# Kernel tuning notes

Measured on AMD Instinct MI355X. Metric: run time of the kernel, lower is better.

Reference implementation:

```python
import jax, jax.numpy as jnp
import numpy as np

T, B, L, I, H = 1024, 1024, 10, 10, 10


def setup_inputs() -> dict:
    key = jax.random.key(0)
    ks = jax.random.split(key, 7)
    scale = 1.0 / np.sqrt(H)
    x = jax.random.normal(ks[0], (T, B, I), dtype=jnp.float32)
    hp = jax.random.normal(ks[1], (L, B, H), dtype=jnp.float32)
    cp = jax.random.normal(ks[2], (L, B, H), dtype=jnp.float32)
    # torch nn.LSTM params, uniform(-1/sqrt(H), 1/sqrt(H)); layer 0 input = I == H so all layers stack
    W_ih = jax.random.uniform(ks[3], (L, 4 * H, I), minval=-scale, maxval=scale, dtype=jnp.float32)
    W_hh = jax.random.uniform(ks[4], (L, 4 * H, H), minval=-scale, maxval=scale, dtype=jnp.float32)
    b_ih = jax.random.uniform(ks[5], (L, 4 * H), minval=-scale, maxval=scale, dtype=jnp.float32)
    b_hh = jax.random.uniform(ks[6], (L, 4 * H), minval=-scale, maxval=scale, dtype=jnp.float32)
    return {"x": x, "hp": hp, "cp": cp, "W_ih": W_ih, "W_hh": W_hh, "b_ih": b_ih, "b_hh": b_hh}


def _run_layer(inp, h0, c0, Wi, Wh, bi, bh):
    # precompute input projections for all timesteps: [T, B, 4H]
    xg = jnp.einsum('tbi,gi->tbg', inp, Wi) + bi + bh

    def step(carry, xg_t):
        h, c = carry
        g = xg_t + h @ Wh.T  # [B, 4H]; torch gate order: i, f, g, o
        i_g, f_g, g_g, o_g = jnp.split(g, 4, axis=-1)
        i_g = jax.nn.sigmoid(i_g)
        f_g = jax.nn.sigmoid(f_g)
        g_g = jnp.tanh(g_g)
        o_g = jax.nn.sigmoid(o_g)
        c = f_g * c + i_g * g_g
        h = o_g * jnp.tanh(c)
        return (h, c), h

    (hT, cT), ys = jax.lax.scan(step, (h0, c0), xg)
    return ys, hT, cT


def reference(x, hp, cp, W_ih, W_hh, b_ih, b_hh):
    out = x
    hns, cns = [], []
    for l in range(hp.shape[0]):  # fixed small layer stack
        out, hn, cn = _run_layer(out, hp[l], cp[l], W_ih[l], W_hh[l], b_ih[l], b_hh[l])
        hns.append(hn)
        cns.append(cn)
    return out, jnp.stack(hns), jnp.stack(cns)
```

## Files before the change

### kernel.cpp

```cpp
#include <hip/hip_runtime.h>

namespace {

constexpr int T = 1024;
constexpr int B = 1024;
constexpr int L = 10;
constexpr int H = 10;
constexpr int NTHREADS = 128;
constexpr int U = 4;
constexpr int NWIN = T / U;
constexpr int NINT = NWIN + L - 1;
constexpr int BH = B * H;
constexpr int ROWF = 20;

using v2f = __attribute__((ext_vector_type(2))) float;
using v4f = __attribute__((ext_vector_type(4))) float;

__device__ __forceinline__ v2f v2fma(v2f a, v2f b, v2f c) {
    return __builtin_elementwise_fma(a, b, c);
}
__device__ __forceinline__ void pin2(v2f& v) { asm volatile("" : "+v"(v)); }
__device__ __forceinline__ float rcp_f(float x) { return __builtin_amdgcn_rcpf(x); }
__device__ __forceinline__ float exp2_f(float x) {
    float r; asm("v_exp_f32 %0, %1" : "=v"(r) : "v"(x)); return r;
}
__device__ __forceinline__ v2f lo2(v4f q) { return __builtin_shufflevector(q, q, 0, 1); }
__device__ __forceinline__ v2f hi2(v4f q) { return __builtin_shufflevector(q, q, 2, 3); }
#define LDS_FENCE asm volatile("" ::: "memory")

__global__
__attribute__((amdgpu_flat_work_group_size(NTHREADS, NTHREADS)))
__attribute__((amdgpu_waves_per_eu(2)))
void lstm_pipeline(const float* __restrict__ x,
                   const float* __restrict__ hp,
                   const float* __restrict__ cp,
                   const float* __restrict__ Wih,
                   const float* __restrict__ Whh,
                   const float* __restrict__ bih,
                   const float* __restrict__ bhh,
                   float* __restrict__ out,
                   float* __restrict__ hn,
                   float* __restrict__ cn)
{
    __shared__ __align__(16) float buf[2][U][L + 1][ROWF];

    const int tid = threadIdx.x;
    const int wv = tid >> 6;
    const int ln = tid & 63;
    int lidx;
    if (wv == 0) lidx = (ln < 60) ? ln : (ln - 10);
    else         lidx = (ln < 40) ? (60 + ln) : (90 + (ln - 40) % 10);
    const int l = lidx / 10;
    const int j = lidx % 10;
    const int b = blockIdx.x;
    const int boff = b * H + j;

    const float NL2E = -1.44269504088896340736f;
    v2f sA; sA[0] = NL2E;        sA[1] = NL2E;
    v2f sB; sB[0] = 2.0f * NL2E; sB[1] = NL2E;
    v2f wiA[10], wiB[10], whA[10], whB[10], bA, bB;
    {
        const float* WiL = Wih + (size_t)l * 4 * H * H;
        const float* WhL = Whh + (size_t)l * 4 * H * H;
        #pragma unroll
        for (int k = 0; k < 10; ++k) {
            v2f t;
            t[0] = WiL[(0 * H + j) * H + k]; t[1] = WiL[(1 * H + j) * H + k];
            wiA[k] = t * sA;
            t[0] = WiL[(2 * H + j) * H + k]; t[1] = WiL[(3 * H + j) * H + k];
            wiB[k] = t * sB;
            t[0] = WhL[(0 * H + j) * H + k]; t[1] = WhL[(1 * H + j) * H + k];
            whA[k] = t * sA;
            t[0] = WhL[(2 * H + j) * H + k]; t[1] = WhL[(3 * H + j) * H + k];
            whB[k] = t * sB;
        }
        const int bo = l * 4 * H;
        bA[0] = bih[bo + j] + bhh[bo + j];
        bA[1] = bih[bo + H + j] + bhh[bo + H + j];
        bB[0] = bih[bo + 2 * H + j] + bhh[bo + 2 * H + j];
        bB[1] = bih[bo + 3 * H + j] + bhh[bo + 3 * H + j];
        bA = bA * sA;
        bB = bB * sB;
    }
    #pragma unroll
    for (int k = 0; k < 10; ++k) { pin2(wiA[k]); pin2(wiB[k]); pin2(whA[k]); pin2(whB[k]); }
    pin2(bA); pin2(bB);

    float h = hp[(l * B + b) * H + j];
    float c = cp[(l * B + b) * H + j];
    {
        v2f hh; hh[0] = h; hh[1] = h;
        *(v2f*)&buf[(l + 1) & 1][U - 1][l + 1][2 * j] = hh;
    }

    const bool is_st = (lidx < 10);
    float xcur[U], xnext[U];
    if (is_st) {
        #pragma unroll
        for (int u = 0; u < U; ++u) {
            float xv = x[(size_t)u * BH + boff];
            v2f xx; xx[0] = xv; xx[1] = xv;
            *(v2f*)&buf[1][u][0][2 * j] = xx;
        }
        #pragma unroll
        for (int u = 0; u < U; ++u) xcur[u] = x[(size_t)(U + u) * BH + boff];
    }
    __syncthreads();

    v2f aA[U], aB[U];

    auto prefetchx = [&](int k) {
        if (is_st && (k + 2) < NWIN) {
            #pragma unroll
            for (int u = 0; u < U; ++u)
                xnext[u] = x[(size_t)((k + 2) * U + u) * BH + boff];
        }
    };

    auto phase1 = [&](int k, int rp) {
        const unsigned w = (unsigned)(k - l);
        if (w < (unsigned)NWIN) {
            #pragma unroll
            for (int u = 0; u < U; ++u) {
                const float* xr = &buf[rp][u][l][0];
                v4f q0 = *(const v4f*)(xr + 0);
                v4f q1 = *(const v4f*)(xr + 4);
                v4f q2 = *(const v4f*)(xr + 8);
                v4f q3 = *(const v4f*)(xr + 12);
                v4f q4 = *(const v4f*)(xr + 16);
                v2f a  = v2fma(wiA[0], lo2(q0), bA);
                v2f bv = v2fma(wiB[0], lo2(q0), bB);
                a = v2fma(wiA[1], hi2(q0), a);  bv = v2fma(wiB[1], hi2(q0), bv);
                a = v2fma(wiA[2], lo2(q1), a);  bv = v2fma(wiB[2], lo2(q1), bv);
                a = v2fma(wiA[3], hi2(q1), a);  bv = v2fma(wiB[3], hi2(q1), bv);
                a = v2fma(wiA[4], lo2(q2), a);  bv = v2fma(wiB[4], lo2(q2), bv);
                a = v2fma(wiA[5], hi2(q2), a);  bv = v2fma(wiB[5], hi2(q2), bv);
                a = v2fma(wiA[6], lo2(q3), a);  bv = v2fma(wiB[6], lo2(q3), bv);
                a = v2fma(wiA[7], hi2(q3), a);  bv = v2fma(wiB[7], hi2(q3), bv);
                a = v2fma(wiA[8], lo2(q4), a);  bv = v2fma(wiB[8], lo2(q4), bv);
                a = v2fma(wiA[9], hi2(q4), a);  bv = v2fma(wiB[9], hi2(q4), bv);
                aA[u] = a;
                aB[u] = bv;
            }
        }
    };

    auto phase2 = [&](int k, int wp, int rp) {
        const unsigned w = (unsigned)(k - l);
        if (w < (unsigned)NWIN) {
            v4f hq0 = *(const v4f*)&buf[rp][U - 1][l + 1][0];
            v4f hq1 = *(const v4f*)&buf[rp][U - 1][l + 1][4];
            v4f hq2 = *(const v4f*)&buf[rp][U - 1][l + 1][8];
            v4f hq3 = *(const v4f*)&buf[rp][U - 1][l + 1][12];
            v4f hq4 = *(const v4f*)&buf[rp][U - 1][l + 1][16];
            float hv[U];
            #pragma unroll
            for (int u = 0; u < U; ++u) {
                v4f q0, q1, q2, q3, q4;
                if (u == 0) { q0 = hq0; q1 = hq1; q2 = hq2; q3 = hq3; q4 = hq4; }
                else {
                    const float* hr = &buf[wp][u - 1][l + 1][0];
                    q0 = *(const v4f*)(hr + 0);
                    q1 = *(const v4f*)(hr + 4);
                    q2 = *(const v4f*)(hr + 8);
                    q3 = *(const v4f*)(hr + 12);
                    q4 = *(const v4f*)(hr + 16);
                }
                v2f a1 = v2fma(whA[0], lo2(q0), aA[u]);
                v2f a2 = whA[1] * hi2(q0);
                v2f b1 = v2fma(whB[0], lo2(q0), aB[u]);
                v2f b2 = whB[1] * hi2(q0);
                a1 = v2fma(whA[2], lo2(q1), a1);  a2 = v2fma(whA[3], hi2(q1), a2);
                b1 = v2fma(whB[2], lo2(q1), b1);  b2 = v2fma(whB[3], hi2(q1), b2);
                a1 = v2fma(whA[4], lo2(q2), a1);  a2 = v2fma(whA[5], hi2(q2), a2);
                b1 = v2fma(whB[4], lo2(q2), b1);  b2 = v2fma(whB[5], hi2(q2), b2);
                a1 = v2fma(whA[6], lo2(q3), a1);  a2 = v2fma(whA[7], hi2(q3), a2);
                b1 = v2fma(whB[6], lo2(q3), b1);  b2 = v2fma(whB[7], hi2(q3), b2);
                a1 = v2fma(whA[8], lo2(q4), a1);  a2 = v2fma(whA[9], hi2(q4), a2);
                b1 = v2fma(whB[8], lo2(q4), b1);  b2 = v2fma(whB[9], hi2(q4), b2);
                const v2f pA = a1 + a2;
                const v2f pB = b1 + b2;
                const float Ei = exp2_f(pA[0]);
                const float Ef = exp2_f(pA[1]);
                const float Eg = exp2_f(pB[0]);
                const float Eo = exp2_f(pB[1]);
                const float d1 = 1.0f + Ef;
                const float e1 = 1.0f + Ei;
                const float e2 = 1.0f + Eg;
                const float d2 = e1 * e2;
                const float num = fmaf(c, d2, (1.0f - Eg) * d1);
                c = num * rcp_f(d1 * d2);
                const float Ec = exp2_f((2.0f * NL2E) * c);
                const float o1 = 1.0f + Eo;
                const float o2 = 1.0f + Ec;
                h = (1.0f - Ec) * rcp_f(o1 * o2);
                v2f hh; hh[0] = h; hh[1] = h;
                *(v2f*)&buf[wp][u][l + 1][2 * j] = hh;
                hv[u] = h;
            }
            if (l == L - 1) {
                const int t0 = (int)w * U;
                #pragma unroll
                for (int u = 0; u < U; ++u)
                    out[(size_t)(t0 + u) * BH + boff] = hv[u];
            }
        }
    };

    auto stagex = [&](int k, int wp) {
        if (is_st && (k + 1) < NWIN) {
            #pragma unroll
            for (int u = 0; u < U; ++u) {
                v2f xx; xx[0] = xcur[u]; xx[1] = xcur[u];
                *(v2f*)&buf[wp][u][0][2 * j] = xx;
            }
            #pragma unroll
            for (int u = 0; u < U; ++u) xcur[u] = xnext[u];
        }
    };

    if (wv == 0) {
        for (int kk = 0; kk < NINT + 1; kk += 2) {
            prefetchx(kk);
            phase1(kk, 1);        LDS_FENCE;
            phase2(kk, 0, 1);     LDS_FENCE;
            stagex(kk, 0);
            __syncthreads();
            prefetchx(kk + 1);
            phase1(kk + 1, 0);    LDS_FENCE;
            phase2(kk + 1, 1, 0); LDS_FENCE;
            stagex(kk + 1, 1);
            __syncthreads();
        }
    } else {
        for (int kk = 0; kk < NINT + 1; kk += 2) {
            phase2(kk - 1, 1, 0); LDS_FENCE;
            phase1(kk, 1);
            __syncthreads();
            phase2(kk, 0, 1);     LDS_FENCE;
            phase1(kk + 1, 0);
            __syncthreads();
        }
    }

    hn[(l * B + b) * H + j] = h;
    cn[(l * B + b) * H + j] = c;
}

}

extern "C" void kernel_launch(void* const* d_in, const int* in_sizes, int n_in,
                              void* d_out, int out_size, void* d_ws, size_t ws_size,
                              hipStream_t stream) {
    (void)in_sizes; (void)n_in; (void)d_ws; (void)ws_size; (void)out_size;
    const float* x   = (const float*)d_in[0];
    const float* hp  = (const float*)d_in[1];
    const float* cp  = (const float*)d_in[2];
    const float* Wih = (const float*)d_in[3];
    const float* Whh = (const float*)d_in[4];
    const float* bih = (const float*)d_in[5];
    const float* bhh = (const float*)d_in[6];

    float* out = (float*)d_out;
    float* hn  = out + (size_t)T * B * H;
    float* cn  = hn + (size_t)L * B * H;

    lstm_pipeline<<<dim3(B), dim3(NTHREADS), 0, stream>>>(
        x, hp, cp, Wih, Whh, bih, bhh, out, hn, cn);
}
```

Before: 484.5 us.

## Store hidden/input rows unduplicated and split dot products along the reduction axis

```diff
diff --git a/kernel.cpp b/kernel.cpp
--- a/kernel.cpp
+++ b/kernel.cpp
@@ -11,7 +11,7 @@
 constexpr int NWIN = T / U;
 constexpr int NINT = NWIN + L - 1;
 constexpr int BH = B * H;
-constexpr int ROWF = 20;
+constexpr int ROWP = 12;
 
 using v2f = __attribute__((ext_vector_type(2))) float;
 using v4f = __attribute__((ext_vector_type(4))) float;
@@ -42,7 +42,7 @@
                    float* __restrict__ hn,
                    float* __restrict__ cn)
 {
-    __shared__ __align__(16) float buf[2][U][L + 1][ROWF];
+    __shared__ __align__(16) float buf[2][U][L + 1][ROWP];
 
     const int tid = threadIdx.x;
     const int wv = tid >> 6;
@@ -56,58 +56,48 @@
     const int boff = b * H + j;
 
     const float NL2E = -1.44269504088896340736f;
-    v2f sA; sA[0] = NL2E;        sA[1] = NL2E;
-    v2f sB; sB[0] = 2.0f * NL2E; sB[1] = NL2E;
-    v2f wiA[10], wiB[10], whA[10], whB[10], bA, bB;
+    v2f wi[4][5], wh[4][5], bias[4];
     {
         const float* WiL = Wih + (size_t)l * 4 * H * H;
         const float* WhL = Whh + (size_t)l * 4 * H * H;
-        #pragma unroll
-        for (int k = 0; k < 10; ++k) {
-            v2f t;
-            t[0] = WiL[(0 * H + j) * H + k]; t[1] = WiL[(1 * H + j) * H + k];
-            wiA[k] = t * sA;
-            t[0] = WiL[(2 * H + j) * H + k]; t[1] = WiL[(3 * H + j) * H + k];
-            wiB[k] = t * sB;
-            t[0] = WhL[(0 * H + j) * H + k]; t[1] = WhL[(1 * H + j) * H + k];
-            whA[k] = t * sA;
-            t[0] = WhL[(2 * H + j) * H + k]; t[1] = WhL[(3 * H + j) * H + k];
-            whB[k] = t * sB;
-        }
         const int bo = l * 4 * H;
-        bA[0] = bih[bo + j] + bhh[bo + j];
-        bA[1] = bih[bo + H + j] + bhh[bo + H + j];
-        bB[0] = bih[bo + 2 * H + j] + bhh[bo + 2 * H + j];
-        bB[1] = bih[bo + 3 * H + j] + bhh[bo + 3 * H + j];
-        bA = bA * sA;
-        bB = bB * sB;
+        #pragma unroll
+        for (int g = 0; g < 4; ++g) {
+            const float s = (g == 2) ? 2.0f * NL2E : NL2E;
+            const float* wr = WiL + (size_t)(g * H + j) * H;
+            const float* hr = WhL + (size_t)(g * H + j) * H;
+            #pragma unroll
+            for (int p = 0; p < 5; ++p) {
+                wi[g][p][0] = wr[2 * p] * s; wi[g][p][1] = wr[2 * p + 1] * s;
+                wh[g][p][0] = hr[2 * p] * s; wh[g][p][1] = hr[2 * p + 1] * s;
+            }
+            bias[g][0] = (bih[bo + g * H + j] + bhh[bo + g * H + j]) * s;
+            bias[g][1] = 0.0f;
+        }
     }
     #pragma unroll
-    for (int k = 0; k < 10; ++k) { pin2(wiA[k]); pin2(wiB[k]); pin2(whA[k]); pin2(whB[k]); }
-    pin2(bA); pin2(bB);
+    for (int g = 0; g < 4; ++g) {
+        #pragma unroll
+        for (int p = 0; p < 5; ++p) { pin2(wi[g][p]); pin2(wh[g][p]); }
+        pin2(bias[g]);
+    }
 
     float h = hp[(l * B + b) * H + j];
     float c = cp[(l * B + b) * H + j];
-    {
-        v2f hh; hh[0] = h; hh[1] = h;
-        *(v2f*)&buf[(l + 1) & 1][U - 1][l + 1][2 * j] = hh;
-    }
+    buf[(l + 1) & 1][U - 1][l + 1][j] = h;
 
     const bool is_st = (lidx < 10);
     float xcur[U], xnext[U];
     if (is_st) {
         #pragma unroll
-        for (int u = 0; u < U; ++u) {
-            float xv = x[(size_t)u * BH + boff];
-            v2f xx; xx[0] = xv; xx[1] = xv;
-            *(v2f*)&buf[1][u][0][2 * j] = xx;
-        }
+        for (int u = 0; u < U; ++u)
+            buf[1][u][0][j] = x[(size_t)u * BH + boff];
         #pragma unroll
         for (int u = 0; u < U; ++u) xcur[u] = x[(size_t)(U + u) * BH + boff];
     }
     __syncthreads();
 
-    v2f aA[U], aB[U];
+    v2f acc[U][4];
 
     auto prefetchx = [&](int k) {
         if (is_st && (k + 2) < NWIN) {
@@ -125,22 +115,16 @@
                 const float* xr = &buf[rp][u][l][0];
                 v4f q0 = *(const v4f*)(xr + 0);
                 v4f q1 = *(const v4f*)(xr + 4);
-                v4f q2 = *(const v4f*)(xr + 8);
-                v4f q3 = *(const v4f*)(xr + 12);
-                v4f q4 = *(const v4f*)(xr + 16);
-                v2f a  = v2fma(wiA[0], lo2(q0), bA);
-                v2f bv = v2fma(wiB[0], lo2(q0), bB);
-                a = v2fma(wiA[1], hi2(q0), a);  bv = v2fma(wiB[1], hi2(q0), bv);
-                a = v2fma(wiA[2], lo2(q1), a);  bv = v2fma(wiB[2], lo2(q1), bv);
-                a = v2fma(wiA[3], hi2(q1), a);  bv = v2fma(wiB[3], hi2(q1), bv);
-                a = v2fma(wiA[4], lo2(q2), a);  bv = v2fma(wiB[4], lo2(q2), bv);
-                a = v2fma(wiA[5], hi2(q2), a);  bv = v2fma(wiB[5], hi2(q2), bv);
-                a = v2fma(wiA[6], lo2(q3), a);  bv = v2fma(wiB[6], lo2(q3), bv);
-                a = v2fma(wiA[7], hi2(q3), a);  bv = v2fma(wiB[7], hi2(q3), bv);
-                a = v2fma(wiA[8], lo2(q4), a);  bv = v2fma(wiB[8], lo2(q4), bv);
-                a = v2fma(wiA[9], hi2(q4), a);  bv = v2fma(wiB[9], hi2(q4), bv);
-                aA[u] = a;
-                aB[u] = bv;
+                v2f q2 = *(const v2f*)(xr + 8);
+                #pragma unroll
+                for (int g = 0; g < 4; ++g) {
+                    v2f a = v2fma(wi[g][0], lo2(q0), bias[g]);
+                    a = v2fma(wi[g][1], hi2(q0), a);
+                    a = v2fma(wi[g][2], lo2(q1), a);
+                    a = v2fma(wi[g][3], hi2(q1), a);
+                    a = v2fma(wi[g][4], q2, a);
+                    acc[u][g] = a;
+                }
             }
         }
     };
@@ -148,42 +132,49 @@
     auto phase2 = [&](int k, int wp, int rp) {
         const unsigned w = (unsigned)(k - l);
         if (w < (unsigned)NWIN) {
-            v4f hq0 = *(const v4f*)&buf[rp][U - 1][l + 1][0];
-            v4f hq1 = *(const v4f*)&buf[rp][U - 1][l + 1][4];
-            v4f hq2 = *(const v4f*)&buf[rp][U - 1][l + 1][8];
-            v4f hq3 = *(const v4f*)&buf[rp][U - 1][l + 1][12];
-            v4f hq4 = *(const v4f*)&buf[rp][U - 1][l + 1][16];
+            const float* hr0 = &buf[rp][U - 1][l + 1][0];
+            v4f hq0 = *(const v4f*)(hr0 + 0);
+            v4f hq1 = *(const v4f*)(hr0 + 4);
+            v2f hq2 = *(const v2f*)(hr0 + 8);
             float hv[U];
             #pragma unroll
             for (int u = 0; u < U; ++u) {
-                v4f q0, q1, q2, q3, q4;
-                if (u == 0) { q0 = hq0; q1 = hq1; q2 = hq2; q3 = hq3; q4 = hq4; }
+                v4f q0, q1; v2f q2;
+                if (u == 0) { q0 = hq0; q1 = hq1; q2 = hq2; }
                 else {
                     const float* hr = &buf[wp][u - 1][l + 1][0];
                     q0 = *(const v4f*)(hr + 0);
                     q1 = *(const v4f*)(hr + 4);
-                    q2 = *(const v4f*)(hr + 8);
-                    q3 = *(const v4f*)(hr + 12);
-                    q4 = *(const v4f*)(hr + 16);
+                    q2 = *(const v2f*)(hr + 8);
                 }
-                v2f a1 = v2fma(whA[0], lo2(q0), aA[u]);
-                v2f a2 = whA[1] * hi2(q0);
-                v2f b1 = v2fma(whB[0], lo2(q0), aB[u]);
-                v2f b2 = whB[1] * hi2(q0);
-                a1 = v2fma(whA[2], lo2(q1), a1);  a2 = v2fma(whA[3], hi2(q1), a2);
-                b1 = v2fma(whB[2], lo2(q1), b1);  b2 = v2fma(whB[3], hi2(q1), b2);
-                a1 = v2fma(whA[4], lo2(q2), a1);  a2 = v2fma(whA[5], hi2(q2), a2);
-                b1 = v2fma(whB[4], lo2(q2), b1);  b2 = v2fma(whB[5], hi2(q2), b2);
-                a1 = v2fma(whA[6], lo2(q3), a1);  a2 = v2fma(whA[7], hi2(q3), a2);
-                b1 = v2fma(whB[6], lo2(q3), b1);  b2 = v2fma(whB[7], hi2(q3), b2);
-                a1 = v2fma(whA[8], lo2(q4), a1);  a2 = v2fma(whA[9], hi2(q4), a2);
-                b1 = v2fma(whB[8], lo2(q4), b1);  b2 = v2fma(whB[9], hi2(q4), b2);
-                const v2f pA = a1 + a2;
-                const v2f pB = b1 + b2;
-                const float Ei = exp2_f(pA[0]);
-                const float Ef = exp2_f(pA[1]);
-                const float Eg = exp2_f(pB[0]);
-                const float Eo = exp2_f(pB[1]);
+                v2f aI = v2fma(wh[0][0], lo2(q0), acc[u][0]);
+                v2f aF = v2fma(wh[1][0], lo2(q0), acc[u][1]);
+                v2f aG = v2fma(wh[2][0], lo2(q0), acc[u][2]);
+                v2f aO = v2fma(wh[3][0], lo2(q0), acc[u][3]);
+                aI = v2fma(wh[0][1], hi2(q0), aI);
+                aF = v2fma(wh[1][1], hi2(q0), aF);
+                aG = v2fma(wh[2][1], hi2(q0), aG);
+                aO = v2fma(wh[3][1], hi2(q0), aO);
+                aI = v2fma(wh[0][2], lo2(q1), aI);
+                aF = v2fma(wh[1][2], lo2(q1), aF);
+                aG = v2fma(wh[2][2], lo2(q1), aG);
+                aO = v2fma(wh[3][2], lo2(q1), aO);
+                aI = v2fma(wh[0][3], hi2(q1), aI);
+                aF = v2fma(wh[1][3], hi2(q1), aF);
+                aG = v2fma(wh[2][3], hi2(q1), aG);
+                aO = v2fma(wh[3][3], hi2(q1), aO);
+                aI = v2fma(wh[0][4], q2, aI);
+                aF = v2fma(wh[1][4], q2, aF);
+                aG = v2fma(wh[2][4], q2, aG);
+                aO = v2fma(wh[3][4], q2, aO);
+                const float pI = aI[0] + aI[1];
+                const float pF = aF[0] + aF[1];
+                const float pG = aG[0] + aG[1];
+                const float pO = aO[0] + aO[1];
+                const float Ei = exp2_f(pI);
+                const float Ef = exp2_f(pF);
+                const float Eg = exp2_f(pG);
+                const float Eo = exp2_f(pO);
                 const float d1 = 1.0f + Ef;
                 const float e1 = 1.0f + Ei;
                 const float e2 = 1.0f + Eg;
@@ -194,8 +185,7 @@
                 const float o1 = 1.0f + Eo;
                 const float o2 = 1.0f + Ec;
                 h = (1.0f - Ec) * rcp_f(o1 * o2);
-                v2f hh; hh[0] = h; hh[1] = h;
-                *(v2f*)&buf[wp][u][l + 1][2 * j] = hh;
+                buf[wp][u][l + 1][j] = h;
                 hv[u] = h;
             }
             if (l == L - 1) {
@@ -210,10 +200,7 @@
     auto stagex = [&](int k, int wp) {
         if (is_st && (k + 1) < NWIN) {
             #pragma unroll
-            for (int u = 0; u < U; ++u) {
-                v2f xx; xx[0] = xcur[u]; xx[1] = xcur[u];
-                *(v2f*)&buf[wp][u][0][2 * j] = xx;
-            }
+            for (int u = 0; u < U; ++u) buf[wp][u][0][j] = xcur[u];
             #pragma unroll
             for (int u = 0; u < U; ++u) xcur[u] = xnext[u];
         }
```

Measured after the change: 459.2 us. 1.06x faster.
